# Kernel optimization log

Hardware: AMD Instinct MI355X
Metric: run time of the kernel (lower is better)

The kernel has to match this reference:

```python
import jax, jax.numpy as jnp
import numpy as np

B, M, H, D, C = 512, 40, 128, 64, 128


def setup_inputs() -> dict:
    key = jax.random.key(0)
    k1, k2, k3, k4 = jax.random.split(key, 4)
    x0 = jax.random.normal(k1, (B, M, D), dtype=jnp.float32)
    xk = jax.random.normal(k2, (B, H, D), dtype=jnp.float32)
    # Conv1d(kernel_size=1) weight [C, H*M, 1] squeezed to [C, H*M]; bias [C]
    W = jax.random.normal(k3, (C, H * M), dtype=jnp.float32) * 0.02
    b = jax.random.normal(k4, (C,), dtype=jnp.float32) * 0.02
    return {"x0": x0, "xk": xk, "W": W, "b": b}


def reference(x0, xk, W, b):
    # torch: outer[b, h*M+m, d] = xk[b,h,d] * x0[b,m,d]; out = conv1d(outer)
    # conv1d with kernel_size=1 is a channel contraction:
    #   out[b,c,d] = sum_{h,m} W[c, h*M+m] * xk[b,h,d] * x0[b,m,d] + b[c]
    Bsz, Hh, Dd = xk.shape
    Mm = x0.shape[1]
    Cc = W.shape[0]
    Wr = W.reshape(Cc, Hh, Mm)  # channel index is h*M + m -> [C, H, M]
    out = jnp.einsum('bhd,bmd,chm->bcd', xk, x0, Wr) + b[None, :, None]
    return out  # [B, C, D]
```

## Files before the change

kernel.cpp:

```cpp
#include <hip/hip_runtime.h>
#include <hip/hip_bf16.h>

typedef __attribute__((ext_vector_type(8))) short short8;
typedef __attribute__((ext_vector_type(4))) float f32x4;
typedef unsigned short u16;
typedef unsigned int u32;

#define NB 512
#define NM 40
#define NH 128
#define ND 64
#define NC 128
#define KTOT 5120

__device__ __forceinline__ u16 f2bf_rne(float f) {
    u32 u = __float_as_uint(f);
    u32 r = u + 0x7FFFu + ((u >> 16) & 1u);
    return (u16)(r >> 16);
}

__global__ void w3_kernel(const float* __restrict__ W, u16* __restrict__ W3) {
    __shared__ u16 kbuf[NH * 20];
    const int c = blockIdx.x >> 1, mh = blockIdx.x & 1;
    const float* src = W + (size_t)c * KTOT + mh * 20;
    for (int i = threadIdx.x; i < NH * 5; i += 256) {
        int h = i / 5, j4 = i % 5;
        float4 v = *(const float4*)(src + h * NM + j4 * 4);
        u16* kb = kbuf + h * 20 + j4 * 4;
        kb[0] = f2bf_rne(v.x); kb[1] = f2bf_rne(v.y);
        kb[2] = f2bf_rne(v.z); kb[3] = f2bf_rne(v.w);
    }
    __syncthreads();
    for (int i = threadIdx.x; i < 320; i += 256) {
        int mo = i >> 4, t = (i >> 2) & 3, q = i & 3;
        int n = (mh * 20 + mo) * 16 + t * 4 + q;
        union { short8 s8; u16 e[8]; } v;
#pragma unroll
        for (int j = 0; j < 8; ++j)
            v.e[j] = kbuf[(t * 32 + q * 8 + j) * 20 + mo];
        *(short8*)(W3 + ((size_t)n * 128 + c) * 8) = v.s8;
    }
}

__global__ void __launch_bounds__(512, 2) cin_main(
    const float* __restrict__ x0g, const float* __restrict__ xkg,
    const float* __restrict__ biasg, const u16* __restrict__ W3,
    float* __restrict__ out)
{
    __shared__ __align__(16) char smem[70144];
    short* xkT    = (short*)smem;
    float* x0s    = (float*)(smem + 34816);
    float* red    = (float*)smem;
    float* bias_s = (float*)(smem + 69632);

    const int tid = threadIdx.x;
    const int w = tid >> 6, L = tid & 63;
    const int q = L >> 4, l16 = L & 15;
    const int bh = (w >> 2) & 1;
    const int rh = (w >> 1) & 1;
    const int mh = w & 1;
    const size_t b0 = 2 * (size_t)blockIdx.x;

    const u16* Ap = W3 + q * 1024 + (size_t)(rh * 64 + l16) * 8;
    const int m0 = mh * 20;

    short8 aP[4][4];
    auto loadAstep = [&](int u2, short8* dst) {
        const size_t m = (size_t)(m0 + (u2 >> 2));
        const int tt = u2 & 3;
        const u16* p = Ap + m * 16384 + tt * 4096;
#pragma unroll
        for (int mt = 0; mt < 4; ++mt)
            dst[mt] = *(const short8*)(p + mt * 128);
    };
    loadAstep(0, aP[0]);
    loadAstep(1, aP[1]);
    loadAstep(2, aP[2]);
    loadAstep(3, aP[3]);

    {
        for (int i = tid; i < 4096; i += 512) {
            int bn = i >> 11, rem = i & 2047;
            int h = rem >> 4, d4 = (rem & 15) << 2;
            float4 v = *(const float4*)(xkg + (b0 + bn) * (NH * ND) + h * ND + d4);
            short* xT = xkT + bn * 8704;
            xT[(d4 + 0) * 136 + h] = (short)f2bf_rne(v.x);
            xT[(d4 + 1) * 136 + h] = (short)f2bf_rne(v.y);
            xT[(d4 + 2) * 136 + h] = (short)f2bf_rne(v.z);
            xT[(d4 + 3) * 136 + h] = (short)f2bf_rne(v.w);
        }
        for (int i = tid; i < 1280; i += 512) {
            int bn = i / 640, rem = i % 640;
            int m = rem >> 4, d4 = (rem & 15) << 2;
            *(f32x4*)(x0s + bn * 2720 + m * 68 + d4) =
                *(const f32x4*)(x0g + (b0 + bn) * (NM * ND) + m * ND + d4);
        }
        if (tid < NC) bias_s[tid] = biasg[tid];
    }
    __syncthreads();

    const float* x0p = x0s + bh * 2720;
    int bofs = bh * 17408 + l16 * 272 + q * 16;

    short8 bB[2][4];
    auto loadB = [&](int tt, short8* dst, int bo) {
        const char* bsrc = (const char*)xkT + bo + tt * 64;
#pragma unroll
        for (int n = 0; n < 4; ++n)
            dst[n] = *(const short8*)(bsrc + n * 4352);
    };
    loadB(0, bB[0], bofs);

    float s[4], sn[4];
#pragma unroll
    for (int n = 0; n < 4; ++n)
        s[n] = x0p[m0 * 68 + n * 16 + l16];

    f32x4 T[4][4] = {};
    f32x4 o[4][4] = {};

    auto body = [&](int u, bool lastB) {
        const int t = u & 3;
        short8* aC = aP[u & 3];
        const short8* bC = bB[u & 1];
        if (!lastB) {
            asm volatile("" : "+v"(bofs));
            loadB((u + 1) & 3, bB[(u + 1) & 1], bofs);
        }
        if (t == 0) {
            const int m = m0 + (u >> 2);
#pragma unroll
            for (int n = 0; n < 4; ++n)
                sn[n] = (m < m0 + 19) ? x0p[(m + 1) * 68 + n * 16 + l16] : 0.f;
        }
#pragma unroll
        for (int n = 0; n < 4; ++n) {
            T[0][n] = __builtin_amdgcn_mfma_f32_16x16x32_bf16(aC[0], bC[n], T[0][n], 0, 0, 0);
            T[1][n] = __builtin_amdgcn_mfma_f32_16x16x32_bf16(aC[1], bC[n], T[1][n], 0, 0, 0);
            T[2][n] = __builtin_amdgcn_mfma_f32_16x16x32_bf16(aC[2], bC[n], T[2][n], 0, 0, 0);
            T[3][n] = __builtin_amdgcn_mfma_f32_16x16x32_bf16(aC[3], bC[n], T[3][n], 0, 0, 0);
        }
        if (u < 76) loadAstep(u + 4, aC);
        if (t == 3) {
#pragma unroll
            for (int n = 0; n < 4; ++n) {
                const float dd = s[n] - sn[n];
#pragma unroll
                for (int mt = 0; mt < 4; ++mt)
                    o[mt][n] += dd * T[mt][n];
                s[n] = sn[n];
            }
        }
    };

#pragma unroll 4
    for (int u = 0; u < 76; ++u)
        body(u, false);
#pragma unroll
    for (int u = 76; u < 80; ++u)
        body(u, u == 79);

    __syncthreads();
    float* myred = red + (bh * 2 + rh) * 4352;
    if (mh == 1) {
#pragma unroll
        for (int mt = 0; mt < 4; ++mt)
#pragma unroll
            for (int n = 0; n < 4; ++n) {
                int d = n * 16 + l16;
                *(f32x4*)(myred + d * 68 + mt * 16 + q * 4) = o[mt][n];
            }
    }
    __syncthreads();
    if (mh == 0) {
        float* op = out + (b0 + bh) * (NC * ND);
#pragma unroll
        for (int mt = 0; mt < 4; ++mt)
#pragma unroll
            for (int n = 0; n < 4; ++n) {
                int d = n * 16 + l16;
                f32x4 r = *(const f32x4*)(myred + d * 68 + mt * 16 + q * 4);
#pragma unroll
                for (int rr = 0; rr < 4; ++rr) {
                    int c = rh * 64 + mt * 16 + q * 4 + rr;
                    op[c * ND + d] = o[mt][n][rr] + r[rr] + bias_s[c];
                }
            }
    }
}

extern "C" void kernel_launch(void* const* d_in, const int* in_sizes, int n_in,
                              void* d_out, int out_size, void* d_ws, size_t ws_size,
                              hipStream_t stream) {
    const float* x0 = (const float*)d_in[0];
    const float* xk = (const float*)d_in[1];
    const float* W  = (const float*)d_in[2];
    const float* bi = (const float*)d_in[3];
    float* out = (float*)d_out;

    u16* W3 = (u16*)d_ws;

    w3_kernel<<<NC * 2, 256, 0, stream>>>(W, W3);
    cin_main<<<NB / 2, 512, 0, stream>>>(x0, xk, bi, W3, out);
}
```

Before: 114.5 us.

## Use one batch per block with per-wave channel split and register-resident B

Restructures the main kernel so each block handles a single batch element, and each of the 8 waves owns 16 output channels over all 40 m values. This removes the cross-wave m-split reduction through shared memory. The whole xk^T tile now stays in registers for the K loop, and shared memory use shrinks so four blocks can fit per CU. In exchange, each wave issues more serial MFMAs with a shallower A prefetch (double buffer). The grid doubles and the W3 weights are reread per batch, so global and L2 traffic for weights goes up.

```diff
diff --git a/kernel.cpp b/kernel.cpp
--- a/kernel.cpp
+++ b/kernel.cpp
@@ -42,150 +42,95 @@
     }
 }
 
-__global__ void __launch_bounds__(512, 2) cin_main(
+__global__ void __launch_bounds__(512, 4) cin_main(
     const float* __restrict__ x0g, const float* __restrict__ xkg,
     const float* __restrict__ biasg, const u16* __restrict__ W3,
     float* __restrict__ out)
 {
-    __shared__ __align__(16) char smem[70144];
+    __shared__ __align__(16) char smem[29824];
     short* xkT    = (short*)smem;
-    float* x0s    = (float*)(smem + 34816);
-    float* red    = (float*)smem;
-    float* bias_s = (float*)(smem + 69632);
+    float* x0s    = (float*)(smem + 18432);
+    float* bias_s = (float*)(smem + 29312);
 
     const int tid = threadIdx.x;
     const int w = tid >> 6, L = tid & 63;
     const int q = L >> 4, l16 = L & 15;
-    const int bh = (w >> 2) & 1;
-    const int rh = (w >> 1) & 1;
-    const int mh = w & 1;
-    const size_t b0 = 2 * (size_t)blockIdx.x;
+    const int rh = w;
+    const size_t b = blockIdx.x;
 
-    const u16* Ap = W3 + q * 1024 + (size_t)(rh * 64 + l16) * 8;
-    const int m0 = mh * 20;
+    const u16* Ap = W3 + q * 1024 + (size_t)(rh * 16 + l16) * 8;
 
-    short8 aP[4][4];
-    auto loadAstep = [&](int u2, short8* dst) {
-        const size_t m = (size_t)(m0 + (u2 >> 2));
-        const int tt = u2 & 3;
-        const u16* p = Ap + m * 16384 + tt * 4096;
-#pragma unroll
-        for (int mt = 0; mt < 4; ++mt)
-            dst[mt] = *(const short8*)(p + mt * 128);
-    };
-    loadAstep(0, aP[0]);
-    loadAstep(1, aP[1]);
-    loadAstep(2, aP[2]);
-    loadAstep(3, aP[3]);
+    short8 aP[2];
+    aP[0] = *(const short8*)(Ap + 0 * 4096);
+    aP[1] = *(const short8*)(Ap + 1 * 4096);
 
-    {
-        for (int i = tid; i < 4096; i += 512) {
-            int bn = i >> 11, rem = i & 2047;
-            int h = rem >> 4, d4 = (rem & 15) << 2;
-            float4 v = *(const float4*)(xkg + (b0 + bn) * (NH * ND) + h * ND + d4);
-            short* xT = xkT + bn * 8704;
-            xT[(d4 + 0) * 136 + h] = (short)f2bf_rne(v.x);
-            xT[(d4 + 1) * 136 + h] = (short)f2bf_rne(v.y);
-            xT[(d4 + 2) * 136 + h] = (short)f2bf_rne(v.z);
-            xT[(d4 + 3) * 136 + h] = (short)f2bf_rne(v.w);
-        }
-        for (int i = tid; i < 1280; i += 512) {
-            int bn = i / 640, rem = i % 640;
-            int m = rem >> 4, d4 = (rem & 15) << 2;
-            *(f32x4*)(x0s + bn * 2720 + m * 68 + d4) =
-                *(const f32x4*)(x0g + (b0 + bn) * (NM * ND) + m * ND + d4);
-        }
-        if (tid < NC) bias_s[tid] = biasg[tid];
+    for (int i = tid; i < 2048; i += 512) {
+        int h = i >> 4, d4 = (i & 15) << 2;
+        float4 v = *(const float4*)(xkg + b * (NH * ND) + h * ND + d4);
+        xkT[(d4 + 0) * 144 + h] = (short)f2bf_rne(v.x);
+        xkT[(d4 + 1) * 144 + h] = (short)f2bf_rne(v.y);
+        xkT[(d4 + 2) * 144 + h] = (short)f2bf_rne(v.z);
+        xkT[(d4 + 3) * 144 + h] = (short)f2bf_rne(v.w);
     }
+    for (int i = tid; i < 640; i += 512) {
+        int m = i >> 4, d4 = (i & 15) << 2;
+        *(f32x4*)(x0s + m * 68 + d4) =
+            *(const f32x4*)(x0g + b * (NM * ND) + m * ND + d4);
+    }
+    if (tid < NC) bias_s[tid] = biasg[tid];
     __syncthreads();
 
-    const float* x0p = x0s + bh * 2720;
-    int bofs = bh * 17408 + l16 * 272 + q * 16;
-
-    short8 bB[2][4];
-    auto loadB = [&](int tt, short8* dst, int bo) {
-        const char* bsrc = (const char*)xkT + bo + tt * 64;
+    const short* Bp = xkT + (size_t)l16 * 144 + q * 8;
+    short8 bR[4][4];
+#pragma unroll
+    for (int t = 0; t < 4; ++t)
 #pragma unroll
         for (int n = 0; n < 4; ++n)
-            dst[n] = *(const short8*)(bsrc + n * 4352);
-    };
-    loadB(0, bB[0], bofs);
+            bR[t][n] = *(const short8*)(Bp + n * (16 * 144) + t * 32);
 
     float s[4], sn[4];
 #pragma unroll
     for (int n = 0; n < 4; ++n)
-        s[n] = x0p[m0 * 68 + n * 16 + l16];
+        s[n] = x0s[n * 16 + l16];
 
-    f32x4 T[4][4] = {};
-    f32x4 o[4][4] = {};
+    f32x4 T[4] = {{0.f,0.f,0.f,0.f},{0.f,0.f,0.f,0.f},{0.f,0.f,0.f,0.f},{0.f,0.f,0.f,0.f}};
+    f32x4 o[4] = {{0.f,0.f,0.f,0.f},{0.f,0.f,0.f,0.f},{0.f,0.f,0.f,0.f},{0.f,0.f,0.f,0.f}};
 
-    auto body = [&](int u, bool lastB) {
+#pragma unroll 4
+    for (int u = 0; u < 160; ++u) {
         const int t = u & 3;
-        short8* aC = aP[u & 3];
-        const short8* bC = bB[u & 1];
-        if (!lastB) {
-            asm volatile("" : "+v"(bofs));
-            loadB((u + 1) & 3, bB[(u + 1) & 1], bofs);
-        }
+        const short8 a = aP[u & 1];
+        const int up = (u + 2 < 160) ? (u + 2) : 159;
+        aP[u & 1] = *(const short8*)(Ap + (size_t)up * 4096);
         if (t == 0) {
-            const int m = m0 + (u >> 2);
+            const int m = u >> 2;
 #pragma unroll
             for (int n = 0; n < 4; ++n)
-                sn[n] = (m < m0 + 19) ? x0p[(m + 1) * 68 + n * 16 + l16] : 0.f;
+                sn[n] = (m < 39) ? x0s[(m + 1) * 68 + n * 16 + l16] : 0.f;
         }
-#pragma unroll
-        for (int n = 0; n < 4; ++n) {
-            T[0][n] = __builtin_amdgcn_mfma_f32_16x16x32_bf16(aC[0], bC[n], T[0][n], 0, 0, 0);
-            T[1][n] = __builtin_amdgcn_mfma_f32_16x16x32_bf16(aC[1], bC[n], T[1][n], 0, 0, 0);
-            T[2][n] = __builtin_amdgcn_mfma_f32_16x16x32_bf16(aC[2], bC[n], T[2][n], 0, 0, 0);
-            T[3][n] = __builtin_amdgcn_mfma_f32_16x16x32_bf16(aC[3], bC[n], T[3][n], 0, 0, 0);
-        }
-        if (u < 76) loadAstep(u + 4, aC);
+        T[0] = __builtin_amdgcn_mfma_f32_16x16x32_bf16(a, bR[t][0], T[0], 0, 0, 0);
+        T[1] = __builtin_amdgcn_mfma_f32_16x16x32_bf16(a, bR[t][1], T[1], 0, 0, 0);
+        T[2] = __builtin_amdgcn_mfma_f32_16x16x32_bf16(a, bR[t][2], T[2], 0, 0, 0);
+        T[3] = __builtin_amdgcn_mfma_f32_16x16x32_bf16(a, bR[t][3], T[3], 0, 0, 0);
         if (t == 3) {
 #pragma unroll
             for (int n = 0; n < 4; ++n) {
                 const float dd = s[n] - sn[n];
-#pragma unroll
-                for (int mt = 0; mt < 4; ++mt)
-                    o[mt][n] += dd * T[mt][n];
+                o[n] += dd * T[n];
                 s[n] = sn[n];
             }
         }
-    };
+    }
 
-#pragma unroll 4
-    for (int u = 0; u < 76; ++u)
-        body(u, false);
+    float* op = out + b * (NC * ND);
 #pragma unroll
-    for (int u = 76; u < 80; ++u)
-        body(u, u == 79);
-
-    __syncthreads();
-    float* myred = red + (bh * 2 + rh) * 4352;
-    if (mh == 1) {
+    for (int n = 0; n < 4; ++n) {
+        const int d = n * 16 + l16;
 #pragma unroll
-        for (int mt = 0; mt < 4; ++mt)
-#pragma unroll
-            for (int n = 0; n < 4; ++n) {
-                int d = n * 16 + l16;
-                *(f32x4*)(myred + d * 68 + mt * 16 + q * 4) = o[mt][n];
-            }
-    }
-    __syncthreads();
-    if (mh == 0) {
-        float* op = out + (b0 + bh) * (NC * ND);
-#pragma unroll
-        for (int mt = 0; mt < 4; ++mt)
-#pragma unroll
-            for (int n = 0; n < 4; ++n) {
-                int d = n * 16 + l16;
-                f32x4 r = *(const f32x4*)(myred + d * 68 + mt * 16 + q * 4);
-#pragma unroll
-                for (int rr = 0; rr < 4; ++rr) {
-                    int c = rh * 64 + mt * 16 + q * 4 + rr;
-                    op[c * ND + d] = o[mt][n][rr] + r[rr] + bias_s[c];
-                }
-            }
+        for (int rr = 0; rr < 4; ++rr) {
+            const int c = rh * 16 + q * 4 + rr;
+            op[c * ND + d] = o[n][rr] + bias_s[c];
+        }
     }
 }
 
@@ -201,5 +146,5 @@
     u16* W3 = (u16*)d_ws;
 
     w3_kernel<<<NC * 2, 256, 0, stream>>>(W, W3);
-    cin_main<<<NB / 2, 512, 0, stream>>>(x0, xk, bi, W3, out);
+    cin_main<<<NB, 512, 0, stream>>>(x0, xk, bi, W3, out);
 }
```

Result: no change. 116.4 us (+1.7%).

## Stage W tiles into shared memory via global_load_lds and reuse across four batches

Applied to the files above, without the earlier changes.

Each block now handles four batches for one half of the output channels, instead of two batches for all channels. The W3 tiles are copied straight from global memory into a double-buffered shared-memory ring with global_load_lds, and all eight waves read them from there. Each wave keeps its xk operand in registers for the whole loop rather than reloading it every step. This is meant to cut redundant global reads of W, but it raises LDS use to about 111 KB, which likely limits the GPU to one block per CU, and adds a full barrier at every m step.

```diff
diff --git a/kernel.cpp b/kernel.cpp
--- a/kernel.cpp
+++ b/kernel.cpp
@@ -17,6 +17,12 @@
     u32 u = __float_as_uint(f);
     u32 r = u + 0x7FFFu + ((u >> 16) & 1u);
     return (u16)(r >> 16);
+}
+
+__device__ __forceinline__ void gload16(const void* g, void* l) {
+    __builtin_amdgcn_global_load_lds(
+        (const __attribute__((address_space(1))) void*)g,
+        (__attribute__((address_space(3))) void*)l, 16, 0, 0);
 }
 
 __global__ void w3_kernel(const float* __restrict__ W, u16* __restrict__ W3) {
@@ -47,121 +53,119 @@
     const float* __restrict__ biasg, const u16* __restrict__ W3,
     float* __restrict__ out)
 {
-    __shared__ __align__(16) char smem[70144];
+    __shared__ __align__(16) char smem[113664];
     short* xkT    = (short*)smem;
-    float* x0s    = (float*)(smem + 34816);
+    char*  ring   = smem;
     float* red    = (float*)smem;
-    float* bias_s = (float*)(smem + 69632);
+    float* x0s    = (float*)(smem + 69632);
+    float* bias_s = (float*)(smem + 113152);
 
     const int tid = threadIdx.x;
     const int w = tid >> 6, L = tid & 63;
     const int q = L >> 4, l16 = L & 15;
-    const int bh = (w >> 2) & 1;
-    const int rh = (w >> 1) & 1;
+    const int bn = w >> 1;
     const int mh = w & 1;
-    const size_t b0 = 2 * (size_t)blockIdx.x;
-
-    const u16* Ap = W3 + q * 1024 + (size_t)(rh * 64 + l16) * 8;
+    const int ch = blockIdx.x & 1;
+    const size_t b0 = 4 * (size_t)(blockIdx.x >> 1);
     const int m0 = mh * 20;
 
-    short8 aP[4][4];
-    auto loadAstep = [&](int u2, short8* dst) {
-        const size_t m = (size_t)(m0 + (u2 >> 2));
-        const int tt = u2 & 3;
-        const u16* p = Ap + m * 16384 + tt * 4096;
-#pragma unroll
-        for (int mt = 0; mt < 4; ++mt)
-            dst[mt] = *(const short8*)(p + mt * 128);
+    const char* W3b = (const char*)W3;
+    u32 srcOff[4];
+#pragma unroll
+    for (int e = 0; e < 4; ++e) {
+        int j = e * 512 + tid;
+        int mhs = j >> 10, jj = j & 1023;
+        int tt = jj >> 8, qq = (jj >> 6) & 3, cc = jj & 63;
+        srcOff[e] = (u32)(((tt * 4 + qq) * 128 + ch * 64 + cc) * 16)
+                  + (u32)mhs * 20u * 32768u;
+    }
+    auto stageM = [&](int lm1, int slot) {
+#pragma unroll
+        for (int e = 0; e < 4; ++e)
+            gload16(W3b + (size_t)(srcOff[e] + (u32)lm1 * 32768u),
+                    ring + slot * 32768 + e * 8192 + tid * 16);
     };
-    loadAstep(0, aP[0]);
-    loadAstep(1, aP[1]);
-    loadAstep(2, aP[2]);
-    loadAstep(3, aP[3]);
-
-    {
-        for (int i = tid; i < 4096; i += 512) {
-            int bn = i >> 11, rem = i & 2047;
-            int h = rem >> 4, d4 = (rem & 15) << 2;
-            float4 v = *(const float4*)(xkg + (b0 + bn) * (NH * ND) + h * ND + d4);
-            short* xT = xkT + bn * 8704;
-            xT[(d4 + 0) * 136 + h] = (short)f2bf_rne(v.x);
-            xT[(d4 + 1) * 136 + h] = (short)f2bf_rne(v.y);
-            xT[(d4 + 2) * 136 + h] = (short)f2bf_rne(v.z);
-            xT[(d4 + 3) * 136 + h] = (short)f2bf_rne(v.w);
-        }
-        for (int i = tid; i < 1280; i += 512) {
-            int bn = i / 640, rem = i % 640;
-            int m = rem >> 4, d4 = (rem & 15) << 2;
-            *(f32x4*)(x0s + bn * 2720 + m * 68 + d4) =
-                *(const f32x4*)(x0g + (b0 + bn) * (NM * ND) + m * ND + d4);
-        }
-        if (tid < NC) bias_s[tid] = biasg[tid];
-    }
-    __syncthreads();
-
-    const float* x0p = x0s + bh * 2720;
-    int bofs = bh * 17408 + l16 * 272 + q * 16;
-
-    short8 bB[2][4];
-    auto loadB = [&](int tt, short8* dst, int bo) {
-        const char* bsrc = (const char*)xkT + bo + tt * 64;
+
+    for (int i = tid; i < 8192; i += 512) {
+        int bi = i >> 11, rem = i & 2047;
+        int h = rem >> 4, d4 = (rem & 15) << 2;
+        float4 v = *(const float4*)(xkg + (b0 + bi) * (NH * ND) + h * ND + d4);
+        short* xT = xkT + bi * 8704;
+        xT[(d4 + 0) * 136 + h] = (short)f2bf_rne(v.x);
+        xT[(d4 + 1) * 136 + h] = (short)f2bf_rne(v.y);
+        xT[(d4 + 2) * 136 + h] = (short)f2bf_rne(v.z);
+        xT[(d4 + 3) * 136 + h] = (short)f2bf_rne(v.w);
+    }
+    for (int i = tid; i < 2560; i += 512) {
+        int bi = i / 640, rem = i % 640;
+        int m = rem >> 4, d4 = (rem & 15) << 2;
+        *(f32x4*)(x0s + bi * 2720 + m * 68 + d4) =
+            *(const f32x4*)(x0g + (b0 + bi) * (NM * ND) + m * ND + d4);
+    }
+    if (tid < NC) bias_s[tid] = biasg[tid];
+    __syncthreads();
+
+    const short* Bp = xkT + bn * 8704 + (size_t)l16 * 136 + q * 8;
+    short8 bR[4][4];
+#pragma unroll
+    for (int t = 0; t < 4; ++t)
 #pragma unroll
         for (int n = 0; n < 4; ++n)
-            dst[n] = *(const short8*)(bsrc + n * 4352);
-    };
-    loadB(0, bB[0], bofs);
-
+            bR[t][n] = *(const short8*)(Bp + n * (16 * 136) + t * 32);
+
+    const float* x0p = x0s + bn * 2720;
     float s[4], sn[4];
 #pragma unroll
     for (int n = 0; n < 4; ++n)
         s[n] = x0p[m0 * 68 + n * 16 + l16];
 
+    __syncthreads();
+    stageM(0, 0);
+    asm volatile("s_waitcnt vmcnt(0)" ::: "memory");
+    __syncthreads();
+
     f32x4 T[4][4] = {};
     f32x4 o[4][4] = {};
 
-    auto body = [&](int u, bool lastB) {
-        const int t = u & 3;
-        short8* aC = aP[u & 3];
-        const short8* bC = bB[u & 1];
-        if (!lastB) {
-            asm volatile("" : "+v"(bofs));
-            loadB((u + 1) & 3, bB[(u + 1) & 1], bofs);
+#pragma unroll 2
+    for (int lm = 0; lm < 20; ++lm) {
+        const int slot = lm & 1;
+        if (lm < 19) stageM(lm + 1, slot ^ 1);
+        const char* tb = ring + slot * 32768 + mh * 16384;
+#pragma unroll
+        for (int t = 0; t < 4; ++t) {
+            short8 aR[4];
+#pragma unroll
+            for (int mt = 0; mt < 4; ++mt)
+                aR[mt] = *(const short8*)(tb + t * 4096 + q * 1024 + (mt * 16 + l16) * 16);
+            if (t == 0) {
+#pragma unroll
+                for (int n = 0; n < 4; ++n)
+                    sn[n] = (lm < 19) ? x0p[(m0 + lm + 1) * 68 + n * 16 + l16] : 0.f;
+            }
+#pragma unroll
+            for (int n = 0; n < 4; ++n) {
+                T[0][n] = __builtin_amdgcn_mfma_f32_16x16x32_bf16(aR[0], bR[t][n], T[0][n], 0, 0, 0);
+                T[1][n] = __builtin_amdgcn_mfma_f32_16x16x32_bf16(aR[1], bR[t][n], T[1][n], 0, 0, 0);
+                T[2][n] = __builtin_amdgcn_mfma_f32_16x16x32_bf16(aR[2], bR[t][n], T[2][n], 0, 0, 0);
+                T[3][n] = __builtin_amdgcn_mfma_f32_16x16x32_bf16(aR[3], bR[t][n], T[3][n], 0, 0, 0);
+            }
+            if (t == 3) {
+#pragma unroll
+                for (int n = 0; n < 4; ++n) {
+                    const float dd = s[n] - sn[n];
+#pragma unroll
+                    for (int mt = 0; mt < 4; ++mt)
+                        o[mt][n] += dd * T[mt][n];
+                    s[n] = sn[n];
+                }
+            }
         }
-        if (t == 0) {
-            const int m = m0 + (u >> 2);
-#pragma unroll
-            for (int n = 0; n < 4; ++n)
-                sn[n] = (m < m0 + 19) ? x0p[(m + 1) * 68 + n * 16 + l16] : 0.f;
-        }
-#pragma unroll
-        for (int n = 0; n < 4; ++n) {
-            T[0][n] = __builtin_amdgcn_mfma_f32_16x16x32_bf16(aC[0], bC[n], T[0][n], 0, 0, 0);
-            T[1][n] = __builtin_amdgcn_mfma_f32_16x16x32_bf16(aC[1], bC[n], T[1][n], 0, 0, 0);
-            T[2][n] = __builtin_amdgcn_mfma_f32_16x16x32_bf16(aC[2], bC[n], T[2][n], 0, 0, 0);
-            T[3][n] = __builtin_amdgcn_mfma_f32_16x16x32_bf16(aC[3], bC[n], T[3][n], 0, 0, 0);
-        }
-        if (u < 76) loadAstep(u + 4, aC);
-        if (t == 3) {
-#pragma unroll
-            for (int n = 0; n < 4; ++n) {
-                const float dd = s[n] - sn[n];
-#pragma unroll
-                for (int mt = 0; mt < 4; ++mt)
-                    o[mt][n] += dd * T[mt][n];
-                s[n] = sn[n];
-            }
-        }
-    };
-
-#pragma unroll 4
-    for (int u = 0; u < 76; ++u)
-        body(u, false);
-#pragma unroll
-    for (int u = 76; u < 80; ++u)
-        body(u, u == 79);
-
-    __syncthreads();
-    float* myred = red + (bh * 2 + rh) * 4352;
+        asm volatile("s_waitcnt vmcnt(0)" ::: "memory");
+        __syncthreads();
+    }
+
+    float* myred = red + bn * 4352;
     if (mh == 1) {
 #pragma unroll
         for (int mt = 0; mt < 4; ++mt)
@@ -173,7 +177,7 @@
     }
     __syncthreads();
     if (mh == 0) {
-        float* op = out + (b0 + bh) * (NC * ND);
+        float* op = out + (b0 + bn) * (NC * ND);
 #pragma unroll
         for (int mt = 0; mt < 4; ++mt)
 #pragma unroll
@@ -182,7 +186,7 @@
                 f32x4 r = *(const f32x4*)(myred + d * 68 + mt * 16 + q * 4);
 #pragma unroll
                 for (int rr = 0; rr < 4; ++rr) {
-                    int c = rh * 64 + mt * 16 + q * 4 + rr;
+                    int c = ch * 64 + mt * 16 + q * 4 + rr;
                     op[c * ND + d] = o[mt][n][rr] + r[rr] + bias_s[c];
                 }
             }
@@ -201,5 +205,5 @@
     u16* W3 = (u16*)d_ws;
 
     w3_kernel<<<NC * 2, 256, 0, stream>>>(W, W3);
-    cin_main<<<NB / 2, 512, 0, stream>>>(x0, xk, bi, W3, out);
-}
+    cin_main<<<256, 512, 0, stream>>>(x0, xk, bi, W3, out);
+}
```

Result: slower. 127.1 us (+11.1%).
